# Kernel tuning notes

Measured on AMD Instinct MI355X. Metric: run time of the kernel, lower is better.

The kernel has to match this reference:

```python
import jax, jax.numpy as jnp
import numpy as np
import math

L, N, D = 1024, 64, 64
O = 1024

def setup_inputs() -> dict:
    key = jax.random.key(0)
    k1, k2 = jax.random.split(key)
    x = jax.random.normal(k1, (L, N, D), dtype=jnp.float32)
    upfold = jax.random.normal(k2, (O, N, D), dtype=jnp.float32)
    return {"x": x, "upfold": upfold}

def reference(x, upfold):
    # x: [L, N, D], upfold: [O, N, D]
    d = x.shape[-1]
    scale = 1.0 / math.sqrt(d)
    # affinities: [L, O, N]
    affinities = jnp.einsum('lnd,ond->lon', x, upfold) * scale
    # weighted sum with (sigmoid - 0.5) weights: [L, N, D]
    features = jnp.einsum('lon,ond->lnd', jax.nn.sigmoid(affinities) - 0.5, upfold)
    return features
```

## Files before the change

### kernel.cpp

```cpp
#include <hip/hip_runtime.h>
#include <stdint.h>

#define ND   4096
#define NST  8
#define BUFB 35840

typedef float    floatx16 __attribute__((ext_vector_type(16)));
typedef _Float16 half8    __attribute__((ext_vector_type(8)));
typedef _Float16 h2       __attribute__((ext_vector_type(2)));
typedef __fp16   fp16x2   __attribute__((ext_vector_type(2)));

__device__ __forceinline__ uint32_t pkh2(float a, float b) {
    fp16x2 p = __builtin_amdgcn_cvt_pkrtz(a, b);
    return __builtin_bit_cast(uint32_t, p);
}

__device__ __forceinline__ half8 mk_frag(uint32_t a, uint32_t b, uint32_t c, uint32_t d) {
    union { uint32_t u[4]; half8 v; } U;
    U.u[0] = a; U.u[1] = b; U.u[2] = c; U.u[3] = d;
    return U.v;
}

__device__ __forceinline__ uint32_t psig(float s0, float s1) {
    const h2 HI = {(_Float16)41.6f,        (_Float16)41.6f};
    const h2 LO = {(_Float16)-41.6f,       (_Float16)-41.6f};
    const h2 SC = {(_Float16)0.0625f,      (_Float16)0.0625f};
    const h2 C0 = {(_Float16)0.03099238f,  (_Float16)0.03099238f};
    const h2 C1 = {(_Float16)-0.00842090f, (_Float16)-0.00842090f};
    const h2 C2 = {(_Float16)0.00151845f,  (_Float16)0.00151845f};
    const h2 C3 = {(_Float16)-1.02197e-4f, (_Float16)-1.02197e-4f};
    h2 s = __builtin_bit_cast(h2, pkh2(s0, s1));
    s = __builtin_elementwise_min(s, HI);
    s = __builtin_elementwise_max(s, LO);
    h2 ha = s * SC;
    h2 v  = ha * ha;
    h2 w  = C2 + v * C3;
    w     = C1 + v * w;
    w     = C0 + v * w;
    h2 f  = s * w;
    return __builtin_bit_cast(uint32_t, f);
}

__global__ void __launch_bounds__(256, 2)
corr_kernel(const float* __restrict__ x, const float* __restrict__ up,
            float* __restrict__ out)
{
    __shared__ __align__(16) uint8_t smem[2 * BUFB];

    const int tid  = threadIdx.x;
    const int lane = tid & 63;
    const int wid  = tid >> 6;
    const int l31  = lane & 31;
    const int h    = lane >> 5;
    const int r8   = tid >> 4;
    const int c    = tid & 15;
    const int n    = blockIdx.x;
    const int lb   = blockIdx.y;
    const int lw   = lb * 128 + wid * 32 + l31;

    const float* ubase = up + (size_t)n * 64;

    float4 va[4], vb[4];
    auto load_super = [&](int st) {
        const float* pr = ubase + (size_t)(st * 128 + 2 * r8) * ND + 4 * c;
        #pragma unroll
        for (int j = 0; j < 4; ++j) {
            va[j] = *(const float4*)(pr + (size_t)(32 * j) * ND);
            vb[j] = *(const float4*)(pr + (size_t)(32 * j) * ND + ND);
        }
    };
    auto stage_super = [&](int b) {
        uint16_t (*Ub)[72]  = (uint16_t (*)[72])(smem + b * BUFB);
        uint32_t (*Ut2)[68] = (uint32_t (*)[68])(smem + b * BUFB + 18432);
        #pragma unroll
        for (int j = 0; j < 4; ++j) {
            *(uint2*)&Ub[2*r8 + 32*j][4*c] =
                make_uint2(pkh2(va[j].x, va[j].y), pkh2(va[j].z, va[j].w));
            *(uint2*)&Ub[2*r8 + 32*j + 1][4*c] =
                make_uint2(pkh2(vb[j].x, vb[j].y), pkh2(vb[j].z, vb[j].w));
            *(uint4*)&Ut2[r8 + 16*j][4*c] =
                make_uint4(pkh2(va[j].x, vb[j].x), pkh2(va[j].y, vb[j].y),
                           pkh2(va[j].z, vb[j].z), pkh2(va[j].w, vb[j].w));
        }
    };

    load_super(0);

    half8 Xf[4];
    {
        float (*Xs)[68] = (float (*)[68])smem;
        const int xr = tid >> 1;
        const int xh = tid & 1;
        const float* xsrc = x + (size_t)(lb * 128 + xr) * ND + n * 64;
        #pragma unroll
        for (int j = 0; j < 8; ++j) {
            const int f4i = xh * 8 + j;
            *(float4*)&Xs[xr][4 * f4i] = *(const float4*)(xsrc + 4 * f4i);
        }
        __syncthreads();
        const int rl = wid * 32 + l31;
        #pragma unroll
        for (int kk = 0; kk < 4; ++kk) {
            float4 f1 = *(const float4*)&Xs[rl][16 * kk + 8 * h];
            float4 f2 = *(const float4*)&Xs[rl][16 * kk + 8 * h + 4];
            Xf[kk] = mk_frag(pkh2(f1.x, f1.y), pkh2(f1.z, f1.w),
                             pkh2(f2.x, f2.y), pkh2(f2.z, f2.w));
        }
        __syncthreads();
    }

    stage_super(0);
    load_super(1);
    __syncthreads();

    floatx16 F0, F1;
    #pragma unroll
    for (int i = 0; i < 16; ++i) { F0[i] = 0.0f; F1[i] = 0.0f; }

    for (int st = 0; st < NST; ++st) {
        const int b = st & 1;
        uint16_t (*Ub)[72] = (uint16_t (*)[72])(smem + b * BUFB);
        const uint32_t* utp = (const uint32_t*)(smem + b * BUFB + 18432);

        half8 A0k[4], A1k[4];
        #pragma unroll
        for (int kk = 0; kk < 4; ++kk) {
            A0k[kk] = *(const half8*)&Ub[l31][16 * kk + 8 * h];
            A1k[kk] = *(const half8*)&Ub[32 + l31][16 * kk + 8 * h];
        }

        if (st + 1 < NST) stage_super(b ^ 1);
        if (st + 2 < NST) load_super(st + 2);

        #pragma unroll
        for (int sub = 0; sub < 2; ++sub) {
            if (sub == 1) {
                #pragma unroll
                for (int kk = 0; kk < 4; ++kk) {
                    A0k[kk] = *(const half8*)&Ub[64 + l31][16 * kk + 8 * h];
                    A1k[kk] = *(const half8*)&Ub[96 + l31][16 * kk + 8 * h];
                }
            }
            floatx16 S0, S1;
            #pragma unroll
            for (int i = 0; i < 16; ++i) { S0[i] = 0.0f; S1[i] = 0.0f; }
            #pragma unroll
            for (int kk = 0; kk < 4; ++kk) {
                S0 = __builtin_amdgcn_mfma_f32_32x32x16_f16(A0k[kk], Xf[kk], S0, 0, 0, 0);
                S1 = __builtin_amdgcn_mfma_f32_32x32x16_f16(A1k[kk], Xf[kk], S1, 0, 0, 0);
            }
            uint32_t P[16];
            #pragma unroll
            for (int m = 0; m < 8; ++m) P[m]     = psig(S0[2*m], S0[2*m+1]);
            #pragma unroll
            for (int m = 0; m < 8; ++m) P[8 + m] = psig(S1[2*m], S1[2*m+1]);
            uint32_t R[8];
            #pragma unroll
            for (int c2 = 0; c2 < 4; ++c2) {
                const uint32_t* Q = P + (c2 >> 1) * 8;
                const int t4 = (c2 & 1) * 4;
                R[2*c2]   = __shfl_xor(h ? Q[t4]     : Q[t4 + 2], 32);
                R[2*c2+1] = __shfl_xor(h ? Q[t4 + 1] : Q[t4 + 3], 32);
            }
            const int obase = 32 * sub;
            #pragma unroll
            for (int c2 = 0; c2 < 4; ++c2) {
                const uint32_t* Q = P + (c2 >> 1) * 8;
                const int t4 = (c2 & 1) * 4;
                half8 B = h ? mk_frag(R[2*c2], R[2*c2+1], Q[t4 + 2], Q[t4 + 3])
                            : mk_frag(Q[t4], Q[t4 + 1], R[2*c2], R[2*c2+1]);
                const int opb = obase + 8 * c2 + 4 * h;
                uint32_t a0[4], a1[4];
                #pragma unroll
                for (int k = 0; k < 4; ++k) {
                    a0[k] = utp[(opb + k) * 68 + l31];
                    a1[k] = utp[(opb + k) * 68 + 32 + l31];
                }
                half8 A0 = mk_frag(a0[0], a0[1], a0[2], a0[3]);
                half8 A1 = mk_frag(a1[0], a1[1], a1[2], a1[3]);
                F0 = __builtin_amdgcn_mfma_f32_32x32x16_f16(A0, B, F0, 0, 0, 0);
                F1 = __builtin_amdgcn_mfma_f32_32x32x16_f16(A1, B, F1, 0, 0, 0);
            }
        }
        __syncthreads();
    }

    float* op = out + (size_t)lw * ND + n * 64;
    #pragma unroll
    for (int q = 0; q < 4; ++q) {
        float4 a; a.x = F0[4*q]; a.y = F0[4*q+1]; a.z = F0[4*q+2]; a.w = F0[4*q+3];
        *(float4*)(op + 8*q + 4*h) = a;
        float4 bq; bq.x = F1[4*q]; bq.y = F1[4*q+1]; bq.z = F1[4*q+2]; bq.w = F1[4*q+3];
        *(float4*)(op + 32 + 8*q + 4*h) = bq;
    }
}

extern "C" void kernel_launch(void* const* d_in, const int* in_sizes, int n_in,
                              void* d_out, int out_size, void* d_ws, size_t ws_size,
                              hipStream_t stream)
{
    const float* x  = (const float*)d_in[0];
    const float* up = (const float*)d_in[1];
    float* out      = (float*)d_out;
    corr_kernel<<<dim3(64, 8), dim3(256), 0, stream>>>(x, up, out);
}
```

Baseline: 102.6 us.

## Process two L row-groups per wave to reuse staged upfold tiles

Each wave now computes 64 output rows (two 32-row groups) sharing the same fp16 upfold tiles and transposed fragments loaded from LDS, halving the grid along L. Transposed-upfold fragments are hoisted into registers before the staging of the next tile. This halves global reads of upfold and LDS fragment loads per output, at the cost of doubled accumulator registers and reduced occupancy (launch bounds lowered to one block per CU, 256 blocks total).

```diff
diff --git a/kernel.cpp b/kernel.cpp
--- a/kernel.cpp
+++ b/kernel.cpp
@@ -41,7 +41,7 @@
     return __builtin_bit_cast(uint32_t, f);
 }
 
-__global__ void __launch_bounds__(256, 2)
+__global__ void __launch_bounds__(256, 1)
 corr_kernel(const float* __restrict__ x, const float* __restrict__ up,
             float* __restrict__ out)
 {
@@ -56,7 +56,6 @@
     const int c    = tid & 15;
     const int n    = blockIdx.x;
     const int lb   = blockIdx.y;
-    const int lw   = lb * 128 + wid * 32 + l31;
 
     const float* ubase = up + (size_t)n * 64;
 
@@ -86,25 +85,26 @@
 
     load_super(0);
 
-    half8 Xf[4];
+    half8 Xf[2][4];
     {
         float (*Xs)[68] = (float (*)[68])smem;
-        const int xr = tid >> 1;
-        const int xh = tid & 1;
-        const float* xsrc = x + (size_t)(lb * 128 + xr) * ND + n * 64;
-        #pragma unroll
-        for (int j = 0; j < 8; ++j) {
-            const int f4i = xh * 8 + j;
-            *(float4*)&Xs[xr][4 * f4i] = *(const float4*)(xsrc + 4 * f4i);
-        }
+        const int m  = tid & 15;
+        const int r0 = tid >> 4;
+        const float* xbase = x + (size_t)(lb * 256 + r0) * ND + n * 64 + 4 * m;
+        #pragma unroll
+        for (int k = 0; k < 16; ++k)
+            *(float4*)&Xs[r0 + 16*k][4*m] = *(const float4*)(xbase + (size_t)(16*k) * ND);
         __syncthreads();
-        const int rl = wid * 32 + l31;
-        #pragma unroll
-        for (int kk = 0; kk < 4; ++kk) {
-            float4 f1 = *(const float4*)&Xs[rl][16 * kk + 8 * h];
-            float4 f2 = *(const float4*)&Xs[rl][16 * kk + 8 * h + 4];
-            Xf[kk] = mk_frag(pkh2(f1.x, f1.y), pkh2(f1.z, f1.w),
-                             pkh2(f2.x, f2.y), pkh2(f2.z, f2.w));
+        #pragma unroll
+        for (int lg = 0; lg < 2; ++lg) {
+            const int rl = wid * 64 + lg * 32 + l31;
+            #pragma unroll
+            for (int kk = 0; kk < 4; ++kk) {
+                float4 f1 = *(const float4*)&Xs[rl][16 * kk + 8 * h];
+                float4 f2 = *(const float4*)&Xs[rl][16 * kk + 8 * h + 4];
+                Xf[lg][kk] = mk_frag(pkh2(f1.x, f1.y), pkh2(f1.z, f1.w),
+                                     pkh2(f2.x, f2.y), pkh2(f2.z, f2.w));
+            }
         }
         __syncthreads();
     }
@@ -113,85 +113,90 @@
     load_super(1);
     __syncthreads();
 
-    floatx16 F0, F1;
+    floatx16 F[2][2];
     #pragma unroll
-    for (int i = 0; i < 16; ++i) { F0[i] = 0.0f; F1[i] = 0.0f; }
+    for (int lg = 0; lg < 2; ++lg)
+        #pragma unroll
+        for (int i = 0; i < 16; ++i) { F[lg][0][i] = 0.0f; F[lg][1][i] = 0.0f; }
 
     for (int st = 0; st < NST; ++st) {
         const int b = st & 1;
         uint16_t (*Ub)[72] = (uint16_t (*)[72])(smem + b * BUFB);
         const uint32_t* utp = (const uint32_t*)(smem + b * BUFB + 18432);
 
-        half8 A0k[4], A1k[4];
-        #pragma unroll
-        for (int kk = 0; kk < 4; ++kk) {
-            A0k[kk] = *(const half8*)&Ub[l31][16 * kk + 8 * h];
-            A1k[kk] = *(const half8*)&Ub[32 + l31][16 * kk + 8 * h];
-        }
-
-        if (st + 1 < NST) stage_super(b ^ 1);
-        if (st + 2 < NST) load_super(st + 2);
-
         #pragma unroll
         for (int sub = 0; sub < 2; ++sub) {
-            if (sub == 1) {
+            const int ob = 64 * sub;
+            half8 A0k[4], A1k[4];
+            #pragma unroll
+            for (int kk = 0; kk < 4; ++kk) {
+                A0k[kk] = *(const half8*)&Ub[ob + l31][16 * kk + 8 * h];
+                A1k[kk] = *(const half8*)&Ub[ob + 32 + l31][16 * kk + 8 * h];
+            }
+            uint32_t ga[4][4], gb[4][4];
+            const int opb0 = 32 * sub + 4 * h;
+            #pragma unroll
+            for (int c2 = 0; c2 < 4; ++c2)
+                #pragma unroll
+                for (int k = 0; k < 4; ++k) {
+                    ga[c2][k] = utp[(opb0 + 8*c2 + k) * 68 + l31];
+                    gb[c2][k] = utp[(opb0 + 8*c2 + k) * 68 + 32 + l31];
+                }
+            if (sub == 0) {
+                if (st + 1 < NST) stage_super(b ^ 1);
+                if (st + 2 < NST) load_super(st + 2);
+            }
+            #pragma unroll
+            for (int lg = 0; lg < 2; ++lg) {
+                floatx16 S0, S1;
+                #pragma unroll
+                for (int i = 0; i < 16; ++i) { S0[i] = 0.0f; S1[i] = 0.0f; }
                 #pragma unroll
                 for (int kk = 0; kk < 4; ++kk) {
-                    A0k[kk] = *(const half8*)&Ub[64 + l31][16 * kk + 8 * h];
-                    A1k[kk] = *(const half8*)&Ub[96 + l31][16 * kk + 8 * h];
-                }
-            }
-            floatx16 S0, S1;
-            #pragma unroll
-            for (int i = 0; i < 16; ++i) { S0[i] = 0.0f; S1[i] = 0.0f; }
-            #pragma unroll
-            for (int kk = 0; kk < 4; ++kk) {
-                S0 = __builtin_amdgcn_mfma_f32_32x32x16_f16(A0k[kk], Xf[kk], S0, 0, 0, 0);
-                S1 = __builtin_amdgcn_mfma_f32_32x32x16_f16(A1k[kk], Xf[kk], S1, 0, 0, 0);
-            }
-            uint32_t P[16];
-            #pragma unroll
-            for (int m = 0; m < 8; ++m) P[m]     = psig(S0[2*m], S0[2*m+1]);
-            #pragma unroll
-            for (int m = 0; m < 8; ++m) P[8 + m] = psig(S1[2*m], S1[2*m+1]);
-            uint32_t R[8];
-            #pragma unroll
-            for (int c2 = 0; c2 < 4; ++c2) {
-                const uint32_t* Q = P + (c2 >> 1) * 8;
-                const int t4 = (c2 & 1) * 4;
-                R[2*c2]   = __shfl_xor(h ? Q[t4]     : Q[t4 + 2], 32);
-                R[2*c2+1] = __shfl_xor(h ? Q[t4 + 1] : Q[t4 + 3], 32);
-            }
-            const int obase = 32 * sub;
-            #pragma unroll
-            for (int c2 = 0; c2 < 4; ++c2) {
-                const uint32_t* Q = P + (c2 >> 1) * 8;
-                const int t4 = (c2 & 1) * 4;
-                half8 B = h ? mk_frag(R[2*c2], R[2*c2+1], Q[t4 + 2], Q[t4 + 3])
-                            : mk_frag(Q[t4], Q[t4 + 1], R[2*c2], R[2*c2+1]);
-                const int opb = obase + 8 * c2 + 4 * h;
-                uint32_t a0[4], a1[4];
-                #pragma unroll
-                for (int k = 0; k < 4; ++k) {
-                    a0[k] = utp[(opb + k) * 68 + l31];
-                    a1[k] = utp[(opb + k) * 68 + 32 + l31];
-                }
-                half8 A0 = mk_frag(a0[0], a0[1], a0[2], a0[3]);
-                half8 A1 = mk_frag(a1[0], a1[1], a1[2], a1[3]);
-                F0 = __builtin_amdgcn_mfma_f32_32x32x16_f16(A0, B, F0, 0, 0, 0);
-                F1 = __builtin_amdgcn_mfma_f32_32x32x16_f16(A1, B, F1, 0, 0, 0);
+                    S0 = __builtin_amdgcn_mfma_f32_32x32x16_f16(A0k[kk], Xf[lg][kk], S0, 0, 0, 0);
+                    S1 = __builtin_amdgcn_mfma_f32_32x32x16_f16(A1k[kk], Xf[lg][kk], S1, 0, 0, 0);
+                }
+                uint32_t P[16];
+                #pragma unroll
+                for (int m = 0; m < 8; ++m) P[m]     = psig(S0[2*m], S0[2*m+1]);
+                #pragma unroll
+                for (int m = 0; m < 8; ++m) P[8 + m] = psig(S1[2*m], S1[2*m+1]);
+                uint32_t R[8];
+                #pragma unroll
+                for (int c2 = 0; c2 < 4; ++c2) {
+                    const uint32_t* Q = P + (c2 >> 1) * 8;
+                    const int t4 = (c2 & 1) * 4;
+                    R[2*c2]   = __shfl_xor(h ? Q[t4]     : Q[t4 + 2], 32);
+                    R[2*c2+1] = __shfl_xor(h ? Q[t4 + 1] : Q[t4 + 3], 32);
+                }
+                #pragma unroll
+                for (int c2 = 0; c2 < 4; ++c2) {
+                    const uint32_t* Q = P + (c2 >> 1) * 8;
+                    const int t4 = (c2 & 1) * 4;
+                    half8 B = h ? mk_frag(R[2*c2], R[2*c2+1], Q[t4 + 2], Q[t4 + 3])
+                                : mk_frag(Q[t4], Q[t4 + 1], R[2*c2], R[2*c2+1]);
+                    half8 A0 = mk_frag(ga[c2][0], ga[c2][1], ga[c2][2], ga[c2][3]);
+                    half8 A1 = mk_frag(gb[c2][0], gb[c2][1], gb[c2][2], gb[c2][3]);
+                    F[lg][0] = __builtin_amdgcn_mfma_f32_32x32x16_f16(A0, B, F[lg][0], 0, 0, 0);
+                    F[lg][1] = __builtin_amdgcn_mfma_f32_32x32x16_f16(A1, B, F[lg][1], 0, 0, 0);
+                }
             }
         }
         __syncthreads();
     }
 
-    float* op = out + (size_t)lw * ND + n * 64;
     #pragma unroll
-    for (int q = 0; q < 4; ++q) {
-        float4 a; a.x = F0[4*q]; a.y = F0[4*q+1]; a.z = F0[4*q+2]; a.w = F0[4*q+3];
-        *(float4*)(op + 8*q + 4*h) = a;
-        float4 bq; bq.x = F1[4*q]; bq.y = F1[4*q+1]; bq.z = F1[4*q+2]; bq.w = F1[4*q+3];
-        *(float4*)(op + 32 + 8*q + 4*h) = bq;
+    for (int lg = 0; lg < 2; ++lg) {
+        float* op = out + (size_t)(lb * 256 + wid * 64 + lg * 32 + l31) * ND + n * 64;
+        #pragma unroll
+        for (int q = 0; q < 4; ++q) {
+            float4 a; a.x = F[lg][0][4*q]; a.y = F[lg][0][4*q+1];
+                      a.z = F[lg][0][4*q+2]; a.w = F[lg][0][4*q+3];
+            *(float4*)(op + 8*q + 4*h) = a;
+            float4 bq; bq.x = F[lg][1][4*q]; bq.y = F[lg][1][4*q+1];
+                       bq.z = F[lg][1][4*q+2]; bq.w = F[lg][1][4*q+3];
+            *(float4*)(op + 32 + 8*q + 4*h) = bq;
+        }
     }
 }
 
@@ -202,5 +207,5 @@
     const float* x  = (const float*)d_in[0];
     const float* up = (const float*)d_in[1];
     float* out      = (float*)d_out;
-    corr_kernel<<<dim3(64, 8), dim3(256), 0, stream>>>(x, up, out);
-}
+    corr_kernel<<<dim3(64, 4), dim3(256), 0, stream>>>(x, up, out);
+}
```

Result: slower. 111.5 us (+8.7%).

## Software-pipeline GEMM1 and GEMM2 across 64-row tiles with transposed LDS layout

Applied to the files above, without the earlier changes.

Shrinks each staged tile from 128 to 64 upfold rows and software-pipelines the loop. Each iteration runs the first GEMM (affinities) for tile t interleaved with the sigmoid-weighted second GEMM for tile t-1, so the two MFMA streams can overlap with the sigmoid VALU work. The transposed copy of upfold in LDS is now stored as a d-major fp16 array, so second-GEMM A fragments load as vector half8 reads instead of scalar dword gathers. The cost is twice as many barriers and more live registers (previous S accumulators and A fragments), which could pressure occupancy at the 2-wave launch bound.

```diff
diff --git a/kernel.cpp b/kernel.cpp
--- a/kernel.cpp
+++ b/kernel.cpp
@@ -2,8 +2,10 @@
 #include <stdint.h>
 
 #define ND   4096
-#define NST  8
-#define BUFB 35840
+#define NT   16
+#define UBB  9216
+#define UTB  16896
+#define BUFB (UBB + UTB)
 
 typedef float    floatx16 __attribute__((ext_vector_type(16)));
 typedef _Float16 half8    __attribute__((ext_vector_type(8)));
@@ -60,31 +62,33 @@
 
     const float* ubase = up + (size_t)n * 64;
 
-    float4 va[4], vb[4];
-    auto load_super = [&](int st) {
-        const float* pr = ubase + (size_t)(st * 128 + 2 * r8) * ND + 4 * c;
-        #pragma unroll
-        for (int j = 0; j < 4; ++j) {
+    float4 va[2], vb[2];
+    auto load_tile = [&](int ot) {
+        const float* pr = ubase + (size_t)(ot * 64 + 2 * r8) * ND + 4 * c;
+        #pragma unroll
+        for (int j = 0; j < 2; ++j) {
             va[j] = *(const float4*)(pr + (size_t)(32 * j) * ND);
             vb[j] = *(const float4*)(pr + (size_t)(32 * j) * ND + ND);
         }
     };
-    auto stage_super = [&](int b) {
-        uint16_t (*Ub)[72]  = (uint16_t (*)[72])(smem + b * BUFB);
-        uint32_t (*Ut2)[68] = (uint32_t (*)[68])(smem + b * BUFB + 18432);
-        #pragma unroll
-        for (int j = 0; j < 4; ++j) {
+    auto stage_tile = [&](int b) {
+        uint16_t (*Ub)[72]   = (uint16_t (*)[72])(smem + b * BUFB);
+        uint16_t (*Ut3)[132] = (uint16_t (*)[132])(smem + b * BUFB + UBB);
+        #pragma unroll
+        for (int j = 0; j < 2; ++j) {
+            const float av[4] = {va[j].x, va[j].y, va[j].z, va[j].w};
+            const float bv[4] = {vb[j].x, vb[j].y, vb[j].z, vb[j].w};
             *(uint2*)&Ub[2*r8 + 32*j][4*c] =
-                make_uint2(pkh2(va[j].x, va[j].y), pkh2(va[j].z, va[j].w));
+                make_uint2(pkh2(av[0], av[1]), pkh2(av[2], av[3]));
             *(uint2*)&Ub[2*r8 + 32*j + 1][4*c] =
-                make_uint2(pkh2(vb[j].x, vb[j].y), pkh2(vb[j].z, vb[j].w));
-            *(uint4*)&Ut2[r8 + 16*j][4*c] =
-                make_uint4(pkh2(va[j].x, vb[j].x), pkh2(va[j].y, vb[j].y),
-                           pkh2(va[j].z, vb[j].z), pkh2(va[j].w, vb[j].w));
+                make_uint2(pkh2(bv[0], bv[1]), pkh2(bv[2], bv[3]));
+            #pragma unroll
+            for (int k = 0; k < 4; ++k)
+                *(uint32_t*)&Ut3[4*c + k][2 * (r8 + 16*j)] = pkh2(av[k], bv[k]);
         }
     };
 
-    load_super(0);
+    load_tile(0);
 
     half8 Xf[4];
     {
@@ -109,52 +113,37 @@
         __syncthreads();
     }
 
-    stage_super(0);
-    load_super(1);
+    stage_tile(0);
+    load_tile(1);
     __syncthreads();
 
     floatx16 F0, F1;
     #pragma unroll
     for (int i = 0; i < 16; ++i) { F0[i] = 0.0f; F1[i] = 0.0f; }
 
-    for (int st = 0; st < NST; ++st) {
-        const int b = st & 1;
-        uint16_t (*Ub)[72] = (uint16_t (*)[72])(smem + b * BUFB);
-        const uint32_t* utp = (const uint32_t*)(smem + b * BUFB + 18432);
-
-        half8 A0k[4], A1k[4];
-        #pragma unroll
-        for (int kk = 0; kk < 4; ++kk) {
-            A0k[kk] = *(const half8*)&Ub[l31][16 * kk + 8 * h];
-            A1k[kk] = *(const half8*)&Ub[32 + l31][16 * kk + 8 * h];
-        }
-
-        if (st + 1 < NST) stage_super(b ^ 1);
-        if (st + 2 < NST) load_super(st + 2);
-
-        #pragma unroll
-        for (int sub = 0; sub < 2; ++sub) {
-            if (sub == 1) {
-                #pragma unroll
-                for (int kk = 0; kk < 4; ++kk) {
-                    A0k[kk] = *(const half8*)&Ub[64 + l31][16 * kk + 8 * h];
-                    A1k[kk] = *(const half8*)&Ub[96 + l31][16 * kk + 8 * h];
-                }
-            }
-            floatx16 S0, S1;
-            #pragma unroll
-            for (int i = 0; i < 16; ++i) { S0[i] = 0.0f; S1[i] = 0.0f; }
+    floatx16 Sp0, Sp1;
+    half8 A2p0[4], A2p1[4];
+
+    for (int t = 0; t <= NT; ++t) {
+        const int b = t & 1;
+        uint16_t (*Ub)[72]   = (uint16_t (*)[72])(smem + b * BUFB);
+        uint16_t (*Ut3)[132] = (uint16_t (*)[132])(smem + b * BUFB + UBB);
+
+        half8 A10[4], A11[4];
+        if (t < NT) {
             #pragma unroll
             for (int kk = 0; kk < 4; ++kk) {
-                S0 = __builtin_amdgcn_mfma_f32_32x32x16_f16(A0k[kk], Xf[kk], S0, 0, 0, 0);
-                S1 = __builtin_amdgcn_mfma_f32_32x32x16_f16(A1k[kk], Xf[kk], S1, 0, 0, 0);
-            }
-            uint32_t P[16];
-            #pragma unroll
-            for (int m = 0; m < 8; ++m) P[m]     = psig(S0[2*m], S0[2*m+1]);
-            #pragma unroll
-            for (int m = 0; m < 8; ++m) P[8 + m] = psig(S1[2*m], S1[2*m+1]);
-            uint32_t R[8];
+                A10[kk] = *(const half8*)&Ub[l31][16 * kk + 8 * h];
+                A11[kk] = *(const half8*)&Ub[32 + l31][16 * kk + 8 * h];
+            }
+        }
+
+        uint32_t P[16], R[8];
+        if (t > 0) {
+            #pragma unroll
+            for (int m = 0; m < 8; ++m) P[m]     = psig(Sp0[2*m], Sp0[2*m+1]);
+            #pragma unroll
+            for (int m = 0; m < 8; ++m) P[8 + m] = psig(Sp1[2*m], Sp1[2*m+1]);
             #pragma unroll
             for (int c2 = 0; c2 < 4; ++c2) {
                 const uint32_t* Q = P + (c2 >> 1) * 8;
@@ -162,27 +151,39 @@
                 R[2*c2]   = __shfl_xor(h ? Q[t4]     : Q[t4 + 2], 32);
                 R[2*c2+1] = __shfl_xor(h ? Q[t4 + 1] : Q[t4 + 3], 32);
             }
-            const int obase = 32 * sub;
+        }
+
+        if (t + 1 < NT) stage_tile(b ^ 1);
+        if (t + 2 < NT) load_tile(t + 2);
+
+        floatx16 S0, S1;
+        #pragma unroll
+        for (int i = 0; i < 16; ++i) { S0[i] = 0.0f; S1[i] = 0.0f; }
+        #pragma unroll
+        for (int u = 0; u < 4; ++u) {
+            if (t < NT) {
+                S0 = __builtin_amdgcn_mfma_f32_32x32x16_f16(A10[u], Xf[u], S0, 0, 0, 0);
+                S1 = __builtin_amdgcn_mfma_f32_32x32x16_f16(A11[u], Xf[u], S1, 0, 0, 0);
+            }
+            if (t > 0) {
+                const uint32_t* Q = P + (u >> 1) * 8;
+                const int t4 = (u & 1) * 4;
+                half8 B = h ? mk_frag(R[2*u], R[2*u+1], Q[t4 + 2], Q[t4 + 3])
+                            : mk_frag(Q[t4], Q[t4 + 1], R[2*u], R[2*u+1]);
+                F0 = __builtin_amdgcn_mfma_f32_32x32x16_f16(A2p0[u], B, F0, 0, 0, 0);
+                F1 = __builtin_amdgcn_mfma_f32_32x32x16_f16(A2p1[u], B, F1, 0, 0, 0);
+            }
+        }
+
+        if (t < NT) {
             #pragma unroll
             for (int c2 = 0; c2 < 4; ++c2) {
-                const uint32_t* Q = P + (c2 >> 1) * 8;
-                const int t4 = (c2 & 1) * 4;
-                half8 B = h ? mk_frag(R[2*c2], R[2*c2+1], Q[t4 + 2], Q[t4 + 3])
-                            : mk_frag(Q[t4], Q[t4 + 1], R[2*c2], R[2*c2+1]);
-                const int opb = obase + 8 * c2 + 4 * h;
-                uint32_t a0[4], a1[4];
-                #pragma unroll
-                for (int k = 0; k < 4; ++k) {
-                    a0[k] = utp[(opb + k) * 68 + l31];
-                    a1[k] = utp[(opb + k) * 68 + 32 + l31];
-                }
-                half8 A0 = mk_frag(a0[0], a0[1], a0[2], a0[3]);
-                half8 A1 = mk_frag(a1[0], a1[1], a1[2], a1[3]);
-                F0 = __builtin_amdgcn_mfma_f32_32x32x16_f16(A0, B, F0, 0, 0, 0);
-                F1 = __builtin_amdgcn_mfma_f32_32x32x16_f16(A1, B, F1, 0, 0, 0);
-            }
-        }
-        __syncthreads();
+                A2p0[c2] = *(const half8*)&Ut3[l31][16 * c2 + 8 * h];
+                A2p1[c2] = *(const half8*)&Ut3[32 + l31][16 * c2 + 8 * h];
+            }
+            Sp0 = S0; Sp1 = S1;
+            __syncthreads();
+        }
     }
 
     float* op = out + (size_t)lw * ND + n * 64;
```

Result: slower. 126.4 us (+23.2%).
